# Performance work log

Measured on AMD Instinct MI355X. Metric: run time of the kernel, lower is better.

## Reference

```python
import jax, jax.numpy as jnp
import numpy as np

N, E, B = 50000, 800000, 64
IN, H, OUT = 64, 128, 64


def _gcn_norm(edge_index, num_nodes):
    # PyG gcn_norm with add_self_loops=True: A_hat = A + I, norm = d^-1/2[src]*d^-1/2[dst]
    loop = jnp.arange(num_nodes)
    src = jnp.concatenate([edge_index[0], loop])
    dst = jnp.concatenate([edge_index[1], loop])
    deg = jax.ops.segment_sum(jnp.ones_like(dst, dtype=jnp.float32), dst,
                              num_segments=num_nodes)  # >= 1 due to self-loops
    dis = deg ** -0.5
    norm = dis[src] * dis[dst]  # [E+N]
    return src, dst, norm


def _gcn_layer(x, W, b, src, dst, norm, num_nodes):
    h = x @ W                                   # linear first (GCNConv order)
    msg = h[src] * norm[:, None]                # gather + normalize, [E+N, H]
    out = jax.ops.segment_sum(msg, dst, num_segments=num_nodes)  # scatter-add
    return out + b


def setup_inputs() -> dict:
    key = jax.random.key(0)
    ks = jax.random.split(key, 12)
    x = jax.random.normal(ks[0], (N, IN), dtype=jnp.float32)
    edge_index = jax.random.randint(ks[1], (2, E), 0, N, dtype=jnp.int64)
    batch = jnp.sort(jax.random.randint(ks[2], (N,), 0, B, dtype=jnp.int64))

    def lin(k, fan_in, fan_out):
        s = 1.0 / np.sqrt(fan_in)
        return jax.random.uniform(k, (fan_in, fan_out), jnp.float32, -s, s)

    return {
        "x": x, "edge_index": edge_index, "batch": batch,
        "W1": lin(ks[3], IN, H), "b1": jnp.zeros((H,), jnp.float32),
        "W2": lin(ks[4], H, H),  "b2": jnp.zeros((H,), jnp.float32),
        "W3": lin(ks[5], H, H),  "b3": jnp.zeros((H,), jnp.float32),
        "W4": lin(ks[6], H, OUT), "b4": jnp.zeros((OUT,), jnp.float32),
    }


def reference(x, edge_index, batch, W1, b1, W2, b2, W3, b3, W4, b4):
    src, dst, norm = _gcn_norm(edge_index, N)
    h = jax.nn.relu(_gcn_layer(x, W1, b1, src, dst, norm, N))
    h = jax.nn.relu(_gcn_layer(h, W2, b2, src, dst, norm, N))
    # global mean pool over graphs
    sums = jax.ops.segment_sum(h, batch, num_segments=B)          # [B, H]
    cnts = jax.ops.segment_sum(jnp.ones((N,), jnp.float32), batch, num_segments=B)
    pooled = sums / jnp.maximum(cnts, 1.0)[:, None]
    # MLP head
    return jax.nn.relu(pooled @ W3 + b3) @ W4 + b4                # [B, OUT]
```

## Files before the change

### kernel.cpp

```cpp
#include <hip/hip_runtime.h>


__device__ __forceinline__ float ldf(const void* p, long long i, int f32) {
    if (f32) return ((const float*)p)[i];
    unsigned int u = ((const unsigned short*)p)[i];
    return __uint_as_float(u << 16);
}
__device__ __forceinline__ float bfl(unsigned int u) { return __uint_as_float(u << 16); }
__device__ __forceinline__ float bfh(unsigned int u) { return __uint_as_float(u & 0xFFFF0000u); }
__device__ __forceinline__ int ld_idx(const int* p, long long i, int i64) {
    return i64 ? p[2 * i] : p[i];
}
__device__ __forceinline__ unsigned short f2bf(float v) {
    unsigned int x = __float_as_uint(v);
    return (unsigned short)((x + 0x7FFFu + ((x >> 16) & 1u)) >> 16);
}
__device__ __forceinline__ int clampi(int v, int lo, int hi) {
    return v < lo ? lo : (v > hi ? hi : v);
}

#define OW1 0
#define OB1 8192
#define OW2 8320
#define OB2 24704
#define OW3 24832
#define OB3 41216
#define OW4 41344
#define OB4 49536
#define OTOT 49600


__global__ void gnn_prep(const void* W1, const void* b1, const void* W2, const void* b2,
                         const void* W3, const void* b3, const void* W4, const void* b4,
                         const void* x, const int* __restrict__ ei,
                         int* __restrict__ flags_out,
                         int* __restrict__ degcnt, float* __restrict__ pooled,
                         float* __restrict__ wsW, unsigned short* __restrict__ xb,
                         int N, int B) {
    __shared__ int s_cnt, s_or;
    const int t = threadIdx.x;
    if (t == 0) { s_cnt = 0; s_or = 0; }
    __syncthreads();
    {
        const unsigned int* w1w = (const unsigned int*)W1;
        int c = 0, o = 0;
        for (int i = t; i < 512; i += 256) {
            unsigned int e = (w1w[i] >> 7) & 0xFFu;
            if (e >= 100 && e <= 140) c++;
        }
        for (int i = t; i < 1024; i += 256) o |= ei[2 * i + 1];
        atomicAdd(&s_cnt, c);
        atomicOr(&s_or, o);
    }
    __syncthreads();
    const int f32 = (s_cnt > 256) ? 0 : 1;
    if (blockIdx.x == 0 && t == 0) {
        flags_out[0] = f32;
        flags_out[1] = (s_or == 0) ? 1 : 0;
    }
    const int i = blockIdx.x * 256 + t;
    const int stride = gridDim.x * 256;
    for (int j = i; j < N; j += stride) degcnt[j] = 0;
    for (int j = i; j < B * 128; j += stride) pooled[j] = 0.f;
    for (int j = i; j < OTOT; j += stride) {
        float v;
        if      (j < OB1) v = ldf(W1, j - OW1, f32);
        else if (j < OW2) v = ldf(b1, j - OB1, f32);
        else if (j < OB2) v = ldf(W2, j - OW2, f32);
        else if (j < OW3) v = ldf(b2, j - OB2, f32);
        else if (j < OB3) v = ldf(W3, j - OW3, f32);
        else if (j < OW4) v = ldf(b3, j - OB3, f32);
        else if (j < OB4) v = ldf(W4, j - OW4, f32);
        else              v = ldf(b4, j - OB4, f32);
        wsW[j] = v;
    }
    if (f32) {
        const float* xf = (const float*)x;
        for (int j = i; j < N * 64; j += stride) xb[j] = f2bf(xf[j]);
    }
}


__global__ void gnn_hist(const int* __restrict__ ei, int E, int N,
                         const int* __restrict__ flags, int* __restrict__ degcnt,
                         int* __restrict__ rank) {
    int base = (blockIdx.x * 256 + threadIdx.x) * 4;
    if (base >= E) return;
    int i64 = flags[1];
    int m = min(4, E - base);
    int d[4], r[4];
#pragma unroll
    for (int j = 0; j < 4; ++j)
        if (j < m) d[j] = clampi(ld_idx(ei, (long long)E + base + j, i64), 0, N - 1);
#pragma unroll
    for (int j = 0; j < 4; ++j)
        if (j < m) r[j] = atomicAdd(&degcnt[d[j]], 1);
#pragma unroll
    for (int j = 0; j < 4; ++j)
        if (j < m) rank[base + j] = r[j];
}

__global__ void gnn_scan1(const int* __restrict__ cnt, int* __restrict__ excl,
                          int* __restrict__ sums, float* __restrict__ dis, int N) {
    __shared__ int sh[256];
    int t = threadIdx.x;
    int i = blockIdx.x * 256 + t;
    int v = (i < N) ? cnt[i] : 0;
    sh[t] = v;
    __syncthreads();
    for (int off = 1; off < 256; off <<= 1) {
        int a = (t >= off) ? sh[t - off] : 0;
        __syncthreads();
        sh[t] += a;
        __syncthreads();
    }
    if (i < N) {
        excl[i] = sh[t] - v;
        dis[i] = rsqrtf((float)v + 1.0f);
    }
    if (t == 255) sums[blockIdx.x] = sh[255];
}

__global__ void gnn_scan2(int* __restrict__ sums, int nb) {
    __shared__ int sh[256];
    int t = threadIdx.x;
    int v = (t < nb) ? sums[t] : 0;
    sh[t] = v;
    __syncthreads();
    for (int off = 1; off < 256; off <<= 1) {
        int a = (t >= off) ? sh[t - off] : 0;
        __syncthreads();
        sh[t] += a;
        __syncthreads();
    }
    if (t < nb) sums[t] = sh[t] - v;
}

template <bool SMALLN>
__global__ void gnn_fill(const int* __restrict__ ei, const int* __restrict__ excl,
                         const int* __restrict__ bsums, const int* __restrict__ rank,
                         void* __restrict__ csr, int E, int N,
                         const int* __restrict__ flags) {
    int e = blockIdx.x * 256 + threadIdx.x;
    if (e >= E) return;
    int i64 = flags[1];
    int s = clampi(ld_idx(ei, (long long)e, i64), 0, N - 1);
    int d = clampi(ld_idx(ei, (long long)E + e, i64), 0, N - 1);
    int pos = excl[d] + bsums[d >> 8] + rank[e];
    if (SMALLN) ((unsigned short*)csr)[pos] = (unsigned short)s;
    else        ((int*)csr)[pos] = s;
}

template <bool SMALLN>
__device__ __forceinline__ int csr_at(const void* csr, int e) {
    return SMALLN ? (int)((const unsigned short*)csr)[e] : ((const int*)csr)[e];
}


template <bool SMALLN>
__global__ __launch_bounds__(128) void gnn_aggx_lin1(const void* __restrict__ x,
                                                     const unsigned short* __restrict__ xconv,
                                                     const int* __restrict__ excl,
                                                     const int* __restrict__ bsums,
                                                     const void* __restrict__ csr,
                                                     const float* __restrict__ dis,
                                                     const int* __restrict__ flags,
                                                     const float* __restrict__ Wf,
                                                     const float* __restrict__ bias,
                                                     int N, int E, float* __restrict__ out) {
    __shared__ float Xs[16 * 64];
    const unsigned int* tab = flags[0] ? (const unsigned int*)xconv : (const unsigned int*)x;
    const int t = threadIdx.x;
    const int nbase = blockIdx.x * 16;
    const int lane = t & 63;
    const int fl = lane & 31;

#pragma unroll
    for (int pass = 0; pass < 4; ++pass) {
        int ln = pass * 4 + (t >> 6) * 2 + (lane >> 5);
        int n = nbase + ln;
        float a0 = 0.f, a1 = 0.f;
        if (n < N) {
            float dn = dis[n], dn2 = dn * dn;
            unsigned int us = tab[(long long)n * 32 + fl];
            a0 = bfl(us) * dn2; a1 = bfh(us) * dn2;
            int beg = excl[n] + bsums[n >> 8];
            int end = (n + 1 < N) ? (excl[n + 1] + bsums[(n + 1) >> 8]) : E;
            int e = beg;
            for (; e + 8 <= end; e += 8) {
                int s0 = csr_at<SMALLN>(csr, e),     s1 = csr_at<SMALLN>(csr, e + 1);
                int s2 = csr_at<SMALLN>(csr, e + 2), s3 = csr_at<SMALLN>(csr, e + 3);
                int s4 = csr_at<SMALLN>(csr, e + 4), s5 = csr_at<SMALLN>(csr, e + 5);
                int s6 = csr_at<SMALLN>(csr, e + 6), s7 = csr_at<SMALLN>(csr, e + 7);
                float w0 = dis[s0], w1 = dis[s1], w2 = dis[s2], w3 = dis[s3];
                float w4 = dis[s4], w5 = dis[s5], w6 = dis[s6], w7 = dis[s7];
                unsigned int u0 = tab[(long long)s0 * 32 + fl];
                unsigned int u1 = tab[(long long)s1 * 32 + fl];
                unsigned int u2 = tab[(long long)s2 * 32 + fl];
                unsigned int u3 = tab[(long long)s3 * 32 + fl];
                unsigned int u4 = tab[(long long)s4 * 32 + fl];
                unsigned int u5 = tab[(long long)s5 * 32 + fl];
                unsigned int u6 = tab[(long long)s6 * 32 + fl];
                unsigned int u7 = tab[(long long)s7 * 32 + fl];
                w0 *= dn; w1 *= dn; w2 *= dn; w3 *= dn;
                w4 *= dn; w5 *= dn; w6 *= dn; w7 *= dn;
                a0 = fmaf(w0, bfl(u0), a0); a1 = fmaf(w0, bfh(u0), a1);
                a0 = fmaf(w1, bfl(u1), a0); a1 = fmaf(w1, bfh(u1), a1);
                a0 = fmaf(w2, bfl(u2), a0); a1 = fmaf(w2, bfh(u2), a1);
                a0 = fmaf(w3, bfl(u3), a0); a1 = fmaf(w3, bfh(u3), a1);
                a0 = fmaf(w4, bfl(u4), a0); a1 = fmaf(w4, bfh(u4), a1);
                a0 = fmaf(w5, bfl(u5), a0); a1 = fmaf(w5, bfh(u5), a1);
                a0 = fmaf(w6, bfl(u6), a0); a1 = fmaf(w6, bfh(u6), a1);
                a0 = fmaf(w7, bfl(u7), a0); a1 = fmaf(w7, bfh(u7), a1);
            }
            for (; e + 4 <= end; e += 4) {
                int s0 = csr_at<SMALLN>(csr, e),     s1 = csr_at<SMALLN>(csr, e + 1);
                int s2 = csr_at<SMALLN>(csr, e + 2), s3 = csr_at<SMALLN>(csr, e + 3);
                float w0 = dis[s0], w1 = dis[s1], w2 = dis[s2], w3 = dis[s3];
                unsigned int u0 = tab[(long long)s0 * 32 + fl];
                unsigned int u1 = tab[(long long)s1 * 32 + fl];
                unsigned int u2 = tab[(long long)s2 * 32 + fl];
                unsigned int u3 = tab[(long long)s3 * 32 + fl];
                w0 *= dn; w1 *= dn; w2 *= dn; w3 *= dn;
                a0 = fmaf(w0, bfl(u0), a0); a1 = fmaf(w0, bfh(u0), a1);
                a0 = fmaf(w1, bfl(u1), a0); a1 = fmaf(w1, bfh(u1), a1);
                a0 = fmaf(w2, bfl(u2), a0); a1 = fmaf(w2, bfh(u2), a1);
                a0 = fmaf(w3, bfl(u3), a0); a1 = fmaf(w3, bfh(u3), a1);
            }
            for (; e < end; ++e) {
                int s = csr_at<SMALLN>(csr, e);
                float w = dis[s] * dn;
                unsigned int u = tab[(long long)s * 32 + fl];
                a0 = fmaf(w, bfl(u), a0); a1 = fmaf(w, bfh(u), a1);
            }
        }
        Xs[ln * 64 + fl * 2]     = a0;
        Xs[ln * 64 + fl * 2 + 1] = a1;
    }
    __syncthreads();

    const int fg = t & 31, ng = t >> 5;
    const int f0 = fg * 4, n0 = ng * 4;
    const float4* Xs4 = (const float4*)Xs;
    const float4* Wp  = (const float4*)Wf;
    float4 acc[4];
#pragma unroll
    for (int j = 0; j < 4; ++j) acc[j] = make_float4(0.f, 0.f, 0.f, 0.f);
#pragma unroll 4
    for (int k4 = 0; k4 < 16; ++k4) {
        const float4 wa = Wp[(4 * k4 + 0) * 32 + fg];
        const float4 wb = Wp[(4 * k4 + 1) * 32 + fg];
        const float4 wc = Wp[(4 * k4 + 2) * 32 + fg];
        const float4 wd = Wp[(4 * k4 + 3) * 32 + fg];
#pragma unroll
        for (int j = 0; j < 4; ++j) {
            const float4 xv = Xs4[(n0 + j) * 16 + k4];
            acc[j].x = fmaf(xv.x, wa.x, acc[j].x); acc[j].y = fmaf(xv.x, wa.y, acc[j].y);
            acc[j].z = fmaf(xv.x, wa.z, acc[j].z); acc[j].w = fmaf(xv.x, wa.w, acc[j].w);
            acc[j].x = fmaf(xv.y, wb.x, acc[j].x); acc[j].y = fmaf(xv.y, wb.y, acc[j].y);
            acc[j].z = fmaf(xv.y, wb.z, acc[j].z); acc[j].w = fmaf(xv.y, wb.w, acc[j].w);
            acc[j].x = fmaf(xv.z, wc.x, acc[j].x); acc[j].y = fmaf(xv.z, wc.y, acc[j].y);
            acc[j].z = fmaf(xv.z, wc.z, acc[j].z); acc[j].w = fmaf(xv.z, wc.w, acc[j].w);
            acc[j].x = fmaf(xv.w, wd.x, acc[j].x); acc[j].y = fmaf(xv.w, wd.y, acc[j].y);
            acc[j].z = fmaf(xv.w, wd.z, acc[j].z); acc[j].w = fmaf(xv.w, wd.w, acc[j].w);
        }
    }
    const float4 b = *(const float4*)&bias[f0];
#pragma unroll
    for (int j = 0; j < 4; ++j) {
        int n = nbase + n0 + j;
        if (n >= N) continue;
        float4 a = acc[j];
        a.x = fmaxf(a.x + b.x, 0.f);
        a.y = fmaxf(a.y + b.y, 0.f);
        a.z = fmaxf(a.z + b.z, 0.f);
        a.w = fmaxf(a.w + b.w, 0.f);
        *(float4*)(out + (long long)n * 128 + f0) = a;
    }
}


template <int K, bool RELU, bool OUTBF>
__global__ __launch_bounds__(128) void gnn_linear(const float* __restrict__ X,
                                                  const float* __restrict__ Wf,
                                                  const float* __restrict__ bias,
                                                  int N, void* __restrict__ out) {
    __shared__ float Xs[16 * K];
    const int t = threadIdx.x;
    const int nbase = blockIdx.x * 16;

#pragma unroll
    for (int it = 0; it < K / 32; ++it) {
        int i4 = t + it * 128;
        int n = nbase + (i4 * 4) / K;
        float4 v = make_float4(0.f, 0.f, 0.f, 0.f);
        if (n < N) v = ((const float4*)X)[(long long)nbase * (K / 4) + i4];
        ((float4*)Xs)[i4] = v;
    }
    __syncthreads();

    const int fg = t & 31, ng = t >> 5;
    const int f0 = fg * 4, n0 = ng * 4;
    const float4* Xs4 = (const float4*)Xs;
    const float4* Wp  = (const float4*)Wf;
    float4 acc[4];
#pragma unroll
    for (int j = 0; j < 4; ++j) acc[j] = make_float4(0.f, 0.f, 0.f, 0.f);
#pragma unroll 4
    for (int k4 = 0; k4 < K / 4; ++k4) {
        const float4 wa = Wp[(4 * k4 + 0) * 32 + fg];
        const float4 wb = Wp[(4 * k4 + 1) * 32 + fg];
        const float4 wc = Wp[(4 * k4 + 2) * 32 + fg];
        const float4 wd = Wp[(4 * k4 + 3) * 32 + fg];
#pragma unroll
        for (int j = 0; j < 4; ++j) {
            const float4 xv = Xs4[(n0 + j) * (K / 4) + k4];
            acc[j].x = fmaf(xv.x, wa.x, acc[j].x); acc[j].y = fmaf(xv.x, wa.y, acc[j].y);
            acc[j].z = fmaf(xv.x, wa.z, acc[j].z); acc[j].w = fmaf(xv.x, wa.w, acc[j].w);
            acc[j].x = fmaf(xv.y, wb.x, acc[j].x); acc[j].y = fmaf(xv.y, wb.y, acc[j].y);
            acc[j].z = fmaf(xv.y, wb.z, acc[j].z); acc[j].w = fmaf(xv.y, wb.w, acc[j].w);
            acc[j].x = fmaf(xv.z, wc.x, acc[j].x); acc[j].y = fmaf(xv.z, wc.y, acc[j].y);
            acc[j].z = fmaf(xv.z, wc.z, acc[j].z); acc[j].w = fmaf(xv.z, wc.w, acc[j].w);
            acc[j].x = fmaf(xv.w, wd.x, acc[j].x); acc[j].y = fmaf(xv.w, wd.y, acc[j].y);
            acc[j].z = fmaf(xv.w, wd.z, acc[j].z); acc[j].w = fmaf(xv.w, wd.w, acc[j].w);
        }
    }
#pragma unroll
    for (int j = 0; j < 4; ++j) {
        int n = nbase + n0 + j;
        if (n >= N) continue;
        float4 a = acc[j];
        if (RELU) {
            const float4 b = *(const float4*)&bias[f0];
            a.x = fmaxf(a.x + b.x, 0.f);
            a.y = fmaxf(a.y + b.y, 0.f);
            a.z = fmaxf(a.z + b.z, 0.f);
            a.w = fmaxf(a.w + b.w, 0.f);
        }
        if (OUTBF) {
            uint2 u;
            u.x = (unsigned int)f2bf(a.x) | ((unsigned int)f2bf(a.y) << 16);
            u.y = (unsigned int)f2bf(a.z) | ((unsigned int)f2bf(a.w) << 16);
            *(uint2*)((unsigned short*)out + (long long)n * 128 + f0) = u;
        } else {
            *(float4*)((float*)out + (long long)n * 128 + f0) = a;
        }
    }
}


template <bool SMALLN>
__global__ __launch_bounds__(256) void gnn_agg_bf(const unsigned short* __restrict__ A2,
                                                  const int* __restrict__ excl,
                                                  const int* __restrict__ bsums,
                                                  const void* __restrict__ csr,
                                                  const float* __restrict__ dis,
                                                  const float* __restrict__ bias,
                                                  float* __restrict__ outC, int N, int E) {
    int t = threadIdx.x;
    int lane = t & 63;
    int n = blockIdx.x * 8 + (t >> 6) * 2 + (lane >> 5);
    if (n >= N) return;
    int fl = lane & 31;
    float dn = dis[n];
    float dn2 = dn * dn;
    uint2 us = *(const uint2*)(A2 + (long long)n * 128 + fl * 4);
    float a0 = bfl(us.x) * dn2, a1 = bfh(us.x) * dn2;
    float a2 = bfl(us.y) * dn2, a3 = bfh(us.y) * dn2;
    int beg = excl[n] + bsums[n >> 8];
    int end = (n + 1 < N) ? (excl[n + 1] + bsums[(n + 1) >> 8]) : E;
    int e = beg;
    for (; e + 8 <= end; e += 8) {
        int s0 = csr_at<SMALLN>(csr, e),     s1 = csr_at<SMALLN>(csr, e + 1);
        int s2 = csr_at<SMALLN>(csr, e + 2), s3 = csr_at<SMALLN>(csr, e + 3);
        int s4 = csr_at<SMALLN>(csr, e + 4), s5 = csr_at<SMALLN>(csr, e + 5);
        int s6 = csr_at<SMALLN>(csr, e + 6), s7 = csr_at<SMALLN>(csr, e + 7);
        float w0 = dis[s0], w1 = dis[s1], w2 = dis[s2], w3 = dis[s3];
        float w4 = dis[s4], w5 = dis[s5], w6 = dis[s6], w7 = dis[s7];
        uint2 u0 = *(const uint2*)(A2 + (long long)s0 * 128 + fl * 4);
        uint2 u1 = *(const uint2*)(A2 + (long long)s1 * 128 + fl * 4);
        uint2 u2 = *(const uint2*)(A2 + (long long)s2 * 128 + fl * 4);
        uint2 u3 = *(const uint2*)(A2 + (long long)s3 * 128 + fl * 4);
        uint2 u4 = *(const uint2*)(A2 + (long long)s4 * 128 + fl * 4);
        uint2 u5 = *(const uint2*)(A2 + (long long)s5 * 128 + fl * 4);
        uint2 u6 = *(const uint2*)(A2 + (long long)s6 * 128 + fl * 4);
        uint2 u7 = *(const uint2*)(A2 + (long long)s7 * 128 + fl * 4);
        w0 *= dn; w1 *= dn; w2 *= dn; w3 *= dn;
        w4 *= dn; w5 *= dn; w6 *= dn; w7 *= dn;
        a0 = fmaf(w0, bfl(u0.x), a0); a1 = fmaf(w0, bfh(u0.x), a1);
        a2 = fmaf(w0, bfl(u0.y), a2); a3 = fmaf(w0, bfh(u0.y), a3);
        a0 = fmaf(w1, bfl(u1.x), a0); a1 = fmaf(w1, bfh(u1.x), a1);
        a2 = fmaf(w1, bfl(u1.y), a2); a3 = fmaf(w1, bfh(u1.y), a3);
        a0 = fmaf(w2, bfl(u2.x), a0); a1 = fmaf(w2, bfh(u2.x), a1);
        a2 = fmaf(w2, bfl(u2.y), a2); a3 = fmaf(w2, bfh(u2.y), a3);
        a0 = fmaf(w3, bfl(u3.x), a0); a1 = fmaf(w3, bfh(u3.x), a1);
        a2 = fmaf(w3, bfl(u3.y), a2); a3 = fmaf(w3, bfh(u3.y), a3);
        a0 = fmaf(w4, bfl(u4.x), a0); a1 = fmaf(w4, bfh(u4.x), a1);
        a2 = fmaf(w4, bfl(u4.y), a2); a3 = fmaf(w4, bfh(u4.y), a3);
        a0 = fmaf(w5, bfl(u5.x), a0); a1 = fmaf(w5, bfh(u5.x), a1);
        a2 = fmaf(w5, bfl(u5.y), a2); a3 = fmaf(w5, bfh(u5.y), a3);
        a0 = fmaf(w6, bfl(u6.x), a0); a1 = fmaf(w6, bfh(u6.x), a1);
        a2 = fmaf(w6, bfl(u6.y), a2); a3 = fmaf(w6, bfh(u6.y), a3);
        a0 = fmaf(w7, bfl(u7.x), a0); a1 = fmaf(w7, bfh(u7.x), a1);
        a2 = fmaf(w7, bfl(u7.y), a2); a3 = fmaf(w7, bfh(u7.y), a3);
    }
    for (; e + 4 <= end; e += 4) {
        int s0 = csr_at<SMALLN>(csr, e),     s1 = csr_at<SMALLN>(csr, e + 1);
        int s2 = csr_at<SMALLN>(csr, e + 2), s3 = csr_at<SMALLN>(csr, e + 3);
        float w0 = dis[s0], w1 = dis[s1], w2 = dis[s2], w3 = dis[s3];
        uint2 u0 = *(const uint2*)(A2 + (long long)s0 * 128 + fl * 4);
        uint2 u1 = *(const uint2*)(A2 + (long long)s1 * 128 + fl * 4);
        uint2 u2 = *(const uint2*)(A2 + (long long)s2 * 128 + fl * 4);
        uint2 u3 = *(const uint2*)(A2 + (long long)s3 * 128 + fl * 4);
        w0 *= dn; w1 *= dn; w2 *= dn; w3 *= dn;
        a0 = fmaf(w0, bfl(u0.x), a0); a1 = fmaf(w0, bfh(u0.x), a1);
        a2 = fmaf(w0, bfl(u0.y), a2); a3 = fmaf(w0, bfh(u0.y), a3);
        a0 = fmaf(w1, bfl(u1.x), a0); a1 = fmaf(w1, bfh(u1.x), a1);
        a2 = fmaf(w1, bfl(u1.y), a2); a3 = fmaf(w1, bfh(u1.y), a3);
        a0 = fmaf(w2, bfl(u2.x), a0); a1 = fmaf(w2, bfh(u2.x), a1);
        a2 = fmaf(w2, bfl(u2.y), a2); a3 = fmaf(w2, bfh(u2.y), a3);
        a0 = fmaf(w3, bfl(u3.x), a0); a1 = fmaf(w3, bfh(u3.x), a1);
        a2 = fmaf(w3, bfl(u3.y), a2); a3 = fmaf(w3, bfh(u3.y), a3);
    }
    for (; e < end; ++e) {
        int s = csr_at<SMALLN>(csr, e);
        float w = dis[s] * dn;
        uint2 u = *(const uint2*)(A2 + (long long)s * 128 + fl * 4);
        a0 = fmaf(w, bfl(u.x), a0); a1 = fmaf(w, bfh(u.x), a1);
        a2 = fmaf(w, bfl(u.y), a2); a3 = fmaf(w, bfh(u.y), a3);
    }
    const float4 b = *(const float4*)&bias[fl * 4];
    float4 o;
    o.x = fmaxf(a0 + b.x, 0.f);
    o.y = fmaxf(a1 + b.y, 0.f);
    o.z = fmaxf(a2 + b.z, 0.f);
    o.w = fmaxf(a3 + b.w, 0.f);
    *(float4*)(outC + (long long)n * 128 + fl * 4) = o;
}


#define PSTRIP 32
__global__ __launch_bounds__(128) void gnn_pool(const float* __restrict__ h,
                                                const int* __restrict__ batch,
                                                const int* __restrict__ flags,
                                                float* __restrict__ pooled, int N, int B) {
    int i64 = flags[1];
    int f = threadIdx.x;
    int n0 = blockIdx.x * PSTRIP;
    if (n0 >= N) return;
    int nend = min(n0 + PSTRIP, N);
    int cur = clampi(ld_idx(batch, n0, i64), 0, B - 1);
    float acc = 0.0f;
    for (int n = n0; n < nend; ++n) {
        int b = clampi(ld_idx(batch, n, i64), 0, B - 1);
        if (b != cur) {
            atomicAdd(&pooled[cur * 128 + f], acc);
            acc = 0.0f; cur = b;
        }
        acc += h[(long long)n * 128 + f];
    }
    atomicAdd(&pooled[cur * 128 + f], acc);
}


__global__ __launch_bounds__(128) void gnn_head(const float* __restrict__ pooled,
                                                const int* __restrict__ batch,
                                                const float* __restrict__ W3,
                                                const float* __restrict__ b3,
                                                const float* __restrict__ W4,
                                                const float* __restrict__ b4,
                                                const int* __restrict__ flags,
                                                void* __restrict__ outv, int N) {
    __shared__ float xs[128];
    __shared__ float rs[128];
    __shared__ float cinv;
    int b = blockIdx.x, f = threadIdx.x;
    if (f == 0) {
        int i64 = flags[1];
        int L = 0, R = N;
        while (L < R) { int m = (L + R) >> 1; if (ld_idx(batch, m, i64) < b) L = m + 1; else R = m; }
        int lo = L;
        L = 0; R = N;
        while (L < R) { int m = (L + R) >> 1; if (ld_idx(batch, m, i64) < b + 1) L = m + 1; else R = m; }
        cinv = 1.0f / fmaxf((float)(L - lo), 1.0f);
    }
    __syncthreads();
    xs[f] = pooled[b * 128 + f] * cinv;
    __syncthreads();
    float acc = b3[f];
    for (int k = 0; k < 128; ++k) acc = fmaf(xs[k], W3[k * 128 + f], acc);
    rs[f] = fmaxf(acc, 0.f);
    __syncthreads();
    if (f < 64) {
        float a2 = b4[f];
        for (int k = 0; k < 128; ++k) a2 = fmaf(rs[k], W4[k * 64 + f], a2);
        if (flags[0]) ((float*)outv)[b * 64 + f] = a2;
        else          ((unsigned short*)outv)[b * 64 + f] = f2bf(a2);
    }
}


extern "C" void kernel_launch(void* const* d_in, const int* in_sizes, int n_in,
                              void* d_out, int out_size, void* d_ws, size_t ws_size,
                              hipStream_t stream) {
    const void* x  = d_in[0];
    const int* ei  = (const int*)d_in[1];
    const int* bat = (const int*)d_in[2];

    const int N = in_sizes[0] / 64;
    const int E = in_sizes[1] / 2;
    const int B = out_size / 64;
    const bool smalln = (N < 65536);

    char* p = (char*)d_ws;
    auto alloc = [&](size_t bytes) { void* q = (void*)p; p += (bytes + 255) & ~(size_t)255; return q; };
    int*   flags    = (int*)alloc(256);
    float* wsW      = (float*)alloc((size_t)OTOT * 4);
    int*   degcnt   = (int*)alloc((size_t)N * 4);
    float* dis      = (float*)alloc((size_t)N * 4);
    int*   excl     = (int*)alloc((size_t)N * 4);
    int*   bsums    = (int*)alloc(1024);
    int*   rank     = (int*)alloc((size_t)E * 4);
    void*  csr      = alloc((size_t)E * (smalln ? 2 : 4));
    unsigned short* xb = (unsigned short*)alloc((size_t)N * 64 * 2);
    float* H1       = (float*)alloc((size_t)N * 128 * 4);
    float* C2       = (float*)alloc((size_t)N * 128 * 4);
    unsigned short* A2 = (unsigned short*)alloc((size_t)N * 128 * 2);
    float* pooled   = (float*)alloc((size_t)B * 128 * 4);
    (void)ws_size; (void)n_in;

    const int nbN = (N + 255) / 256;

    gnn_prep<<<512, 256, 0, stream>>>(d_in[3], d_in[4], d_in[5], d_in[6],
                                      d_in[7], d_in[8], d_in[9], d_in[10],
                                      x, ei, flags, degcnt, pooled, wsW, xb, N, B);

    gnn_hist<<<(E + 1023) / 1024, 256, 0, stream>>>(ei, E, N, flags, degcnt, rank);
    gnn_scan1<<<nbN, 256, 0, stream>>>(degcnt, excl, bsums, dis, N);
    gnn_scan2<<<1, 256, 0, stream>>>(bsums, nbN);
    if (smalln)
        gnn_fill<true><<<(E + 255) / 256, 256, 0, stream>>>(ei, excl, bsums, rank, csr, E, N, flags);
    else
        gnn_fill<false><<<(E + 255) / 256, 256, 0, stream>>>(ei, excl, bsums, rank, csr, E, N, flags);

    const int nlin = (N + 15) / 16;
    const int nagg = (N + 7) / 8;

    if (smalln)
        gnn_aggx_lin1<true><<<nlin, 128, 0, stream>>>(x, xb, excl, bsums, csr, dis, flags,
                                                      wsW + OW1, wsW + OB1, N, E, H1);
    else
        gnn_aggx_lin1<false><<<nlin, 128, 0, stream>>>(x, xb, excl, bsums, csr, dis, flags,
                                                       wsW + OW1, wsW + OB1, N, E, H1);

    gnn_linear<128, false, true><<<nlin, 128, 0, stream>>>(H1, wsW + OW2, wsW + OB2, N, (void*)A2);
    if (smalln)
        gnn_agg_bf<true><<<nagg, 256, 0, stream>>>(A2, excl, bsums, csr, dis, wsW + OB2, C2, N, E);
    else
        gnn_agg_bf<false><<<nagg, 256, 0, stream>>>(A2, excl, bsums, csr, dis, wsW + OB2, C2, N, E);

    gnn_pool<<<(N + PSTRIP - 1) / PSTRIP, 128, 0, stream>>>(C2, bat, flags, pooled, N, B);
    gnn_head<<<B, 128, 0, stream>>>(pooled, bat, wsW + OW3, wsW + OB3,
                                    wsW + OW4, wsW + OB4, flags, d_out, N);
}
```

Before: 272.8 us.

## Pre-scale source rows by inverse sqrt degree and parallelize edge gathers across lanes

Source features are now multiplied by dis[src] once per node: during x-to-bf16 conversion in the fill kernel, and in the layer-2 linear epilogue. The aggregation kernels can then sum plain rows and apply dis[dst] once at the end, which removes the per-edge dis[s] gather and multiply. The aggregation loops now split edges across lane groups with 16-byte vector loads, then combine partial sums with xor shuffles, which gives more memory-level parallelism per node. Rounding the pre-scaled values to bf16 changes numerics slightly, and the x conversion now runs unconditionally inside the fill kernel.

```diff
diff --git a/kernel.cpp b/kernel.cpp
--- a/kernel.cpp
+++ b/kernel.cpp
@@ -32,11 +32,10 @@
 
 __global__ void gnn_prep(const void* W1, const void* b1, const void* W2, const void* b2,
                          const void* W3, const void* b3, const void* W4, const void* b4,
-                         const void* x, const int* __restrict__ ei,
+                         const int* __restrict__ ei,
                          int* __restrict__ flags_out,
                          int* __restrict__ degcnt, float* __restrict__ pooled,
-                         float* __restrict__ wsW, unsigned short* __restrict__ xb,
-                         int N, int B) {
+                         float* __restrict__ wsW, int N, int B) {
     __shared__ int s_cnt, s_or;
     const int t = threadIdx.x;
     if (t == 0) { s_cnt = 0; s_or = 0; }
@@ -74,10 +73,6 @@
         else              v = ldf(b4, j - OB4, f32);
         wsW[j] = v;
     }
-    if (f32) {
-        const float* xf = (const float*)x;
-        for (int j = i; j < N * 64; j += stride) xb[j] = f2bf(xf[j]);
-    }
 }
 
 
@@ -140,15 +135,37 @@
 __global__ void gnn_fill(const int* __restrict__ ei, const int* __restrict__ excl,
                          const int* __restrict__ bsums, const int* __restrict__ rank,
                          void* __restrict__ csr, int E, int N,
-                         const int* __restrict__ flags) {
-    int e = blockIdx.x * 256 + threadIdx.x;
-    if (e >= E) return;
-    int i64 = flags[1];
-    int s = clampi(ld_idx(ei, (long long)e, i64), 0, N - 1);
-    int d = clampi(ld_idx(ei, (long long)E + e, i64), 0, N - 1);
-    int pos = excl[d] + bsums[d >> 8] + rank[e];
-    if (SMALLN) ((unsigned short*)csr)[pos] = (unsigned short)s;
-    else        ((int*)csr)[pos] = s;
+                         const int* __restrict__ flags,
+                         const void* __restrict__ x, const float* __restrict__ dis,
+                         unsigned short* __restrict__ xb) {
+    const int tid = blockIdx.x * 256 + threadIdx.x;
+    const int i64 = flags[1];
+    if (tid < E) {
+        int s = clampi(ld_idx(ei, (long long)tid, i64), 0, N - 1);
+        int d = clampi(ld_idx(ei, (long long)E + tid, i64), 0, N - 1);
+        int pos = excl[d] + bsums[d >> 8] + rank[tid];
+        if (SMALLN) ((unsigned short*)csr)[pos] = (unsigned short)s;
+        else        ((int*)csr)[pos] = s;
+    }
+    const int f32 = flags[0];
+    const int total = N * 16;
+    const int stride = gridDim.x * 256;
+    for (int j = tid; j < total; j += stride) {
+        int n = j >> 4;
+        float dn = dis[n];
+        float v0, v1, v2, v3;
+        if (f32) {
+            float4 xv = ((const float4*)x)[j];
+            v0 = xv.x; v1 = xv.y; v2 = xv.z; v3 = xv.w;
+        } else {
+            ushort4 xv = ((const ushort4*)x)[j];
+            v0 = bfl(xv.x); v1 = bfl(xv.y); v2 = bfl(xv.z); v3 = bfl(xv.w);
+        }
+        ushort4 o;
+        o.x = f2bf(v0 * dn); o.y = f2bf(v1 * dn);
+        o.z = f2bf(v2 * dn); o.w = f2bf(v3 * dn);
+        ((ushort4*)xb)[j] = o;
+    }
 }
 
 template <bool SMALLN>
@@ -158,89 +175,62 @@
 
 
 template <bool SMALLN>
-__global__ __launch_bounds__(128) void gnn_aggx_lin1(const void* __restrict__ x,
-                                                     const unsigned short* __restrict__ xconv,
+__global__ __launch_bounds__(128) void gnn_aggx_lin1(const unsigned short* __restrict__ xb,
                                                      const int* __restrict__ excl,
                                                      const int* __restrict__ bsums,
                                                      const void* __restrict__ csr,
                                                      const float* __restrict__ dis,
-                                                     const int* __restrict__ flags,
                                                      const float* __restrict__ Wf,
                                                      const float* __restrict__ bias,
                                                      int N, int E, float* __restrict__ out) {
     __shared__ float Xs[16 * 64];
-    const unsigned int* tab = flags[0] ? (const unsigned int*)xconv : (const unsigned int*)x;
     const int t = threadIdx.x;
     const int nbase = blockIdx.x * 16;
+    const int wave = t >> 6;
     const int lane = t & 63;
-    const int fl = lane & 31;
-
-#pragma unroll
-    for (int pass = 0; pass < 4; ++pass) {
-        int ln = pass * 4 + (t >> 6) * 2 + (lane >> 5);
-        int n = nbase + ln;
-        float a0 = 0.f, a1 = 0.f;
+    const int eslot = lane >> 3;
+    const int fg = lane & 7;
+
+    for (int pass = 0; pass < 8; ++pass) {
+        const int ln = pass * 2 + wave;
+        const int n = nbase + ln;
+        float a0 = 0.f, a1 = 0.f, a2 = 0.f, a3 = 0.f;
+        float a4 = 0.f, a5 = 0.f, a6 = 0.f, a7 = 0.f;
         if (n < N) {
-            float dn = dis[n], dn2 = dn * dn;
-            unsigned int us = tab[(long long)n * 32 + fl];
-            a0 = bfl(us) * dn2; a1 = bfh(us) * dn2;
             int beg = excl[n] + bsums[n >> 8];
             int end = (n + 1 < N) ? (excl[n + 1] + bsums[(n + 1) >> 8]) : E;
-            int e = beg;
-            for (; e + 8 <= end; e += 8) {
-                int s0 = csr_at<SMALLN>(csr, e),     s1 = csr_at<SMALLN>(csr, e + 1);
-                int s2 = csr_at<SMALLN>(csr, e + 2), s3 = csr_at<SMALLN>(csr, e + 3);
-                int s4 = csr_at<SMALLN>(csr, e + 4), s5 = csr_at<SMALLN>(csr, e + 5);
-                int s6 = csr_at<SMALLN>(csr, e + 6), s7 = csr_at<SMALLN>(csr, e + 7);
-                float w0 = dis[s0], w1 = dis[s1], w2 = dis[s2], w3 = dis[s3];
-                float w4 = dis[s4], w5 = dis[s5], w6 = dis[s6], w7 = dis[s7];
-                unsigned int u0 = tab[(long long)s0 * 32 + fl];
-                unsigned int u1 = tab[(long long)s1 * 32 + fl];
-                unsigned int u2 = tab[(long long)s2 * 32 + fl];
-                unsigned int u3 = tab[(long long)s3 * 32 + fl];
-                unsigned int u4 = tab[(long long)s4 * 32 + fl];
-                unsigned int u5 = tab[(long long)s5 * 32 + fl];
-                unsigned int u6 = tab[(long long)s6 * 32 + fl];
-                unsigned int u7 = tab[(long long)s7 * 32 + fl];
-                w0 *= dn; w1 *= dn; w2 *= dn; w3 *= dn;
-                w4 *= dn; w5 *= dn; w6 *= dn; w7 *= dn;
-                a0 = fmaf(w0, bfl(u0), a0); a1 = fmaf(w0, bfh(u0), a1);
-                a0 = fmaf(w1, bfl(u1), a0); a1 = fmaf(w1, bfh(u1), a1);
-                a0 = fmaf(w2, bfl(u2), a0); a1 = fmaf(w2, bfh(u2), a1);
-                a0 = fmaf(w3, bfl(u3), a0); a1 = fmaf(w3, bfh(u3), a1);
-                a0 = fmaf(w4, bfl(u4), a0); a1 = fmaf(w4, bfh(u4), a1);
-                a0 = fmaf(w5, bfl(u5), a0); a1 = fmaf(w5, bfh(u5), a1);
-                a0 = fmaf(w6, bfl(u6), a0); a1 = fmaf(w6, bfh(u6), a1);
-                a0 = fmaf(w7, bfl(u7), a0); a1 = fmaf(w7, bfh(u7), a1);
+            for (int e = beg + eslot; e < end; e += 8) {
+                int s = csr_at<SMALLN>(csr, e);
+                uint4 u = *(const uint4*)(xb + (long long)s * 64 + fg * 8);
+                a0 += bfl(u.x); a1 += bfh(u.x);
+                a2 += bfl(u.y); a3 += bfh(u.y);
+                a4 += bfl(u.z); a5 += bfh(u.z);
+                a6 += bfl(u.w); a7 += bfh(u.w);
             }
-            for (; e + 4 <= end; e += 4) {
-                int s0 = csr_at<SMALLN>(csr, e),     s1 = csr_at<SMALLN>(csr, e + 1);
-                int s2 = csr_at<SMALLN>(csr, e + 2), s3 = csr_at<SMALLN>(csr, e + 3);
-                float w0 = dis[s0], w1 = dis[s1], w2 = dis[s2], w3 = dis[s3];
-                unsigned int u0 = tab[(long long)s0 * 32 + fl];
-                unsigned int u1 = tab[(long long)s1 * 32 + fl];
-                unsigned int u2 = tab[(long long)s2 * 32 + fl];
-                unsigned int u3 = tab[(long long)s3 * 32 + fl];
-                w0 *= dn; w1 *= dn; w2 *= dn; w3 *= dn;
-                a0 = fmaf(w0, bfl(u0), a0); a1 = fmaf(w0, bfh(u0), a1);
-                a0 = fmaf(w1, bfl(u1), a0); a1 = fmaf(w1, bfh(u1), a1);
-                a0 = fmaf(w2, bfl(u2), a0); a1 = fmaf(w2, bfh(u2), a1);
-                a0 = fmaf(w3, bfl(u3), a0); a1 = fmaf(w3, bfh(u3), a1);
-            }
-            for (; e < end; ++e) {
-                int s = csr_at<SMALLN>(csr, e);
-                float w = dis[s] * dn;
-                unsigned int u = tab[(long long)s * 32 + fl];
-                a0 = fmaf(w, bfl(u), a0); a1 = fmaf(w, bfh(u), a1);
-            }
-        }
-        Xs[ln * 64 + fl * 2]     = a0;
-        Xs[ln * 64 + fl * 2 + 1] = a1;
-    }
-    __syncthreads();
-
-    const int fg = t & 31, ng = t >> 5;
-    const int f0 = fg * 4, n0 = ng * 4;
+        }
+#pragma unroll
+        for (int m = 8; m <= 32; m <<= 1) {
+            a0 += __shfl_xor(a0, m); a1 += __shfl_xor(a1, m);
+            a2 += __shfl_xor(a2, m); a3 += __shfl_xor(a3, m);
+            a4 += __shfl_xor(a4, m); a5 += __shfl_xor(a5, m);
+            a6 += __shfl_xor(a6, m); a7 += __shfl_xor(a7, m);
+        }
+        if (n < N && eslot == 0) {
+            float dn = dis[n];
+            uint4 u = *(const uint4*)(xb + (long long)n * 64 + fg * 8);
+            float4 o0, o1;
+            o0.x = (a0 + bfl(u.x)) * dn; o0.y = (a1 + bfh(u.x)) * dn;
+            o0.z = (a2 + bfl(u.y)) * dn; o0.w = (a3 + bfh(u.y)) * dn;
+            o1.x = (a4 + bfl(u.z)) * dn; o1.y = (a5 + bfh(u.z)) * dn;
+            o1.z = (a6 + bfl(u.w)) * dn; o1.w = (a7 + bfh(u.w)) * dn;
+            *(float4*)&Xs[ln * 64 + fg * 8]     = o0;
+            *(float4*)&Xs[ln * 64 + fg * 8 + 4] = o1;
+        }
+    }
+    __syncthreads();
+
+    const int fgB = t & 31, ng = t >> 5;
+    const int f0 = fgB * 4, n0 = ng * 4;
     const float4* Xs4 = (const float4*)Xs;
     const float4* Wp  = (const float4*)Wf;
     float4 acc[4];
@@ -248,10 +238,10 @@
     for (int j = 0; j < 4; ++j) acc[j] = make_float4(0.f, 0.f, 0.f, 0.f);
 #pragma unroll 4
     for (int k4 = 0; k4 < 16; ++k4) {
-        const float4 wa = Wp[(4 * k4 + 0) * 32 + fg];
-        const float4 wb = Wp[(4 * k4 + 1) * 32 + fg];
-        const float4 wc = Wp[(4 * k4 + 2) * 32 + fg];
-        const float4 wd = Wp[(4 * k4 + 3) * 32 + fg];
+        const float4 wa = Wp[(4 * k4 + 0) * 32 + fgB];
+        const float4 wb = Wp[(4 * k4 + 1) * 32 + fgB];
+        const float4 wc = Wp[(4 * k4 + 2) * 32 + fgB];
+        const float4 wd = Wp[(4 * k4 + 3) * 32 + fgB];
 #pragma unroll
         for (int j = 0; j < 4; ++j) {
             const float4 xv = Xs4[(n0 + j) * 16 + k4];
@@ -284,6 +274,7 @@
 __global__ __launch_bounds__(128) void gnn_linear(const float* __restrict__ X,
                                                   const float* __restrict__ Wf,
                                                   const float* __restrict__ bias,
+                                                  const float* __restrict__ dis,
                                                   int N, void* __restrict__ out) {
     __shared__ float Xs[16 * K];
     const int t = threadIdx.x;
@@ -338,6 +329,8 @@
             a.w = fmaxf(a.w + b.w, 0.f);
         }
         if (OUTBF) {
+            const float dn = dis[n];
+            a.x *= dn; a.y *= dn; a.z *= dn; a.w *= dn;
             uint2 u;
             u.x = (unsigned int)f2bf(a.x) | ((unsigned int)f2bf(a.y) << 16);
             u.y = (unsigned int)f2bf(a.z) | ((unsigned int)f2bf(a.w) << 16);
@@ -357,85 +350,48 @@
                                                   const float* __restrict__ dis,
                                                   const float* __restrict__ bias,
                                                   float* __restrict__ outC, int N, int E) {
-    int t = threadIdx.x;
-    int lane = t & 63;
-    int n = blockIdx.x * 8 + (t >> 6) * 2 + (lane >> 5);
+    const int t = threadIdx.x;
+    const int lane = t & 63;
+    const int n = blockIdx.x * 4 + (t >> 6);
     if (n >= N) return;
-    int fl = lane & 31;
-    float dn = dis[n];
-    float dn2 = dn * dn;
-    uint2 us = *(const uint2*)(A2 + (long long)n * 128 + fl * 4);
-    float a0 = bfl(us.x) * dn2, a1 = bfh(us.x) * dn2;
-    float a2 = bfl(us.y) * dn2, a3 = bfh(us.y) * dn2;
+    const int eslot = lane >> 4;
+    const int fg = lane & 15;
+    float a0 = 0.f, a1 = 0.f, a2 = 0.f, a3 = 0.f;
+    float a4 = 0.f, a5 = 0.f, a6 = 0.f, a7 = 0.f;
     int beg = excl[n] + bsums[n >> 8];
     int end = (n + 1 < N) ? (excl[n + 1] + bsums[(n + 1) >> 8]) : E;
-    int e = beg;
-    for (; e + 8 <= end; e += 8) {
-        int s0 = csr_at<SMALLN>(csr, e),     s1 = csr_at<SMALLN>(csr, e + 1);
-        int s2 = csr_at<SMALLN>(csr, e + 2), s3 = csr_at<SMALLN>(csr, e + 3);
-        int s4 = csr_at<SMALLN>(csr, e + 4), s5 = csr_at<SMALLN>(csr, e + 5);
-        int s6 = csr_at<SMALLN>(csr, e + 6), s7 = csr_at<SMALLN>(csr, e + 7);
-        float w0 = dis[s0], w1 = dis[s1], w2 = dis[s2], w3 = dis[s3];
-        float w4 = dis[s4], w5 = dis[s5], w6 = dis[s6], w7 = dis[s7];
-        uint2 u0 = *(const uint2*)(A2 + (long long)s0 * 128 + fl * 4);
-        uint2 u1 = *(const uint2*)(A2 + (long long)s1 * 128 + fl * 4);
-        uint2 u2 = *(const uint2*)(A2 + (long long)s2 * 128 + fl * 4);
-        uint2 u3 = *(const uint2*)(A2 + (long long)s3 * 128 + fl * 4);
-        uint2 u4 = *(const uint2*)(A2 + (long long)s4 * 128 + fl * 4);
-        uint2 u5 = *(const uint2*)(A2 + (long long)s5 * 128 + fl * 4);
-        uint2 u6 = *(const uint2*)(A2 + (long long)s6 * 128 + fl * 4);
-        uint2 u7 = *(const uint2*)(A2 + (long long)s7 * 128 + fl * 4);
-        w0 *= dn; w1 *= dn; w2 *= dn; w3 *= dn;
-        w4 *= dn; w5 *= dn; w6 *= dn; w7 *= dn;
-        a0 = fmaf(w0, bfl(u0.x), a0); a1 = fmaf(w0, bfh(u0.x), a1);
-        a2 = fmaf(w0, bfl(u0.y), a2); a3 = fmaf(w0, bfh(u0.y), a3);
-        a0 = fmaf(w1, bfl(u1.x), a0); a1 = fmaf(w1, bfh(u1.x), a1);
-        a2 = fmaf(w1, bfl(u1.y), a2); a3 = fmaf(w1, bfh(u1.y), a3);
-        a0 = fmaf(w2, bfl(u2.x), a0); a1 = fmaf(w2, bfh(u2.x), a1);
-        a2 = fmaf(w2, bfl(u2.y), a2); a3 = fmaf(w2, bfh(u2.y), a3);
-        a0 = fmaf(w3, bfl(u3.x), a0); a1 = fmaf(w3, bfh(u3.x), a1);
-        a2 = fmaf(w3, bfl(u3.y), a2); a3 = fmaf(w3, bfh(u3.y), a3);
-        a0 = fmaf(w4, bfl(u4.x), a0); a1 = fmaf(w4, bfh(u4.x), a1);
-        a2 = fmaf(w4, bfl(u4.y), a2); a3 = fmaf(w4, bfh(u4.y), a3);
-        a0 = fmaf(w5, bfl(u5.x), a0); a1 = fmaf(w5, bfh(u5.x), a1);
-        a2 = fmaf(w5, bfl(u5.y), a2); a3 = fmaf(w5, bfh(u5.y), a3);
-        a0 = fmaf(w6, bfl(u6.x), a0); a1 = fmaf(w6, bfh(u6.x), a1);
-        a2 = fmaf(w6, bfl(u6.y), a2); a3 = fmaf(w6, bfh(u6.y), a3);
-        a0 = fmaf(w7, bfl(u7.x), a0); a1 = fmaf(w7, bfh(u7.x), a1);
-        a2 = fmaf(w7, bfl(u7.y), a2); a3 = fmaf(w7, bfh(u7.y), a3);
-    }
-    for (; e + 4 <= end; e += 4) {
-        int s0 = csr_at<SMALLN>(csr, e),     s1 = csr_at<SMALLN>(csr, e + 1);
-        int s2 = csr_at<SMALLN>(csr, e + 2), s3 = csr_at<SMALLN>(csr, e + 3);
-        float w0 = dis[s0], w1 = dis[s1], w2 = dis[s2], w3 = dis[s3];
-        uint2 u0 = *(const uint2*)(A2 + (long long)s0 * 128 + fl * 4);
-        uint2 u1 = *(const uint2*)(A2 + (long long)s1 * 128 + fl * 4);
-        uint2 u2 = *(const uint2*)(A2 + (long long)s2 * 128 + fl * 4);
-        uint2 u3 = *(const uint2*)(A2 + (long long)s3 * 128 + fl * 4);
-        w0 *= dn; w1 *= dn; w2 *= dn; w3 *= dn;
-        a0 = fmaf(w0, bfl(u0.x), a0); a1 = fmaf(w0, bfh(u0.x), a1);
-        a2 = fmaf(w0, bfl(u0.y), a2); a3 = fmaf(w0, bfh(u0.y), a3);
-        a0 = fmaf(w1, bfl(u1.x), a0); a1 = fmaf(w1, bfh(u1.x), a1);
-        a2 = fmaf(w1, bfl(u1.y), a2); a3 = fmaf(w1, bfh(u1.y), a3);
-        a0 = fmaf(w2, bfl(u2.x), a0); a1 = fmaf(w2, bfh(u2.x), a1);
-        a2 = fmaf(w2, bfl(u2.y), a2); a3 = fmaf(w2, bfh(u2.y), a3);
-        a0 = fmaf(w3, bfl(u3.x), a0); a1 = fmaf(w3, bfh(u3.x), a1);
-        a2 = fmaf(w3, bfl(u3.y), a2); a3 = fmaf(w3, bfh(u3.y), a3);
-    }
-    for (; e < end; ++e) {
+    for (int e = beg + eslot; e < end; e += 4) {
         int s = csr_at<SMALLN>(csr, e);
-        float w = dis[s] * dn;
-        uint2 u = *(const uint2*)(A2 + (long long)s * 128 + fl * 4);
-        a0 = fmaf(w, bfl(u.x), a0); a1 = fmaf(w, bfh(u.x), a1);
-        a2 = fmaf(w, bfl(u.y), a2); a3 = fmaf(w, bfh(u.y), a3);
-    }
-    const float4 b = *(const float4*)&bias[fl * 4];
-    float4 o;
-    o.x = fmaxf(a0 + b.x, 0.f);
-    o.y = fmaxf(a1 + b.y, 0.f);
-    o.z = fmaxf(a2 + b.z, 0.f);
-    o.w = fmaxf(a3 + b.w, 0.f);
-    *(float4*)(outC + (long long)n * 128 + fl * 4) = o;
+        uint4 u = *(const uint4*)(A2 + (long long)s * 128 + fg * 8);
+        a0 += bfl(u.x); a1 += bfh(u.x);
+        a2 += bfl(u.y); a3 += bfh(u.y);
+        a4 += bfl(u.z); a5 += bfh(u.z);
+        a6 += bfl(u.w); a7 += bfh(u.w);
+    }
+#pragma unroll
+    for (int m = 16; m <= 32; m <<= 1) {
+        a0 += __shfl_xor(a0, m); a1 += __shfl_xor(a1, m);
+        a2 += __shfl_xor(a2, m); a3 += __shfl_xor(a3, m);
+        a4 += __shfl_xor(a4, m); a5 += __shfl_xor(a5, m);
+        a6 += __shfl_xor(a6, m); a7 += __shfl_xor(a7, m);
+    }
+    if (lane < 16) {
+        float dn = dis[n];
+        uint4 u = *(const uint4*)(A2 + (long long)n * 128 + fg * 8);
+        const float4 bA = *(const float4*)&bias[fg * 8];
+        const float4 bB = *(const float4*)&bias[fg * 8 + 4];
+        float4 o0, o1;
+        o0.x = fmaxf((a0 + bfl(u.x)) * dn + bA.x, 0.f);
+        o0.y = fmaxf((a1 + bfh(u.x)) * dn + bA.y, 0.f);
+        o0.z = fmaxf((a2 + bfl(u.y)) * dn + bA.z, 0.f);
+        o0.w = fmaxf((a3 + bfh(u.y)) * dn + bA.w, 0.f);
+        o1.x = fmaxf((a4 + bfl(u.z)) * dn + bB.x, 0.f);
+        o1.y = fmaxf((a5 + bfh(u.z)) * dn + bB.y, 0.f);
+        o1.z = fmaxf((a6 + bfl(u.w)) * dn + bB.z, 0.f);
+        o1.w = fmaxf((a7 + bfh(u.w)) * dn + bB.w, 0.f);
+        *(float4*)(outC + (long long)n * 128 + fg * 8)     = o0;
+        *(float4*)(outC + (long long)n * 128 + fg * 8 + 4) = o1;
+    }
 }
 
 
@@ -533,27 +489,29 @@
 
     gnn_prep<<<512, 256, 0, stream>>>(d_in[3], d_in[4], d_in[5], d_in[6],
                                       d_in[7], d_in[8], d_in[9], d_in[10],
-                                      x, ei, flags, degcnt, pooled, wsW, xb, N, B);
+                                      ei, flags, degcnt, pooled, wsW, N, B);
 
     gnn_hist<<<(E + 1023) / 1024, 256, 0, stream>>>(ei, E, N, flags, degcnt, rank);
     gnn_scan1<<<nbN, 256, 0, stream>>>(degcnt, excl, bsums, dis, N);
     gnn_scan2<<<1, 256, 0, stream>>>(bsums, nbN);
     if (smalln)
-        gnn_fill<true><<<(E + 255) / 256, 256, 0, stream>>>(ei, excl, bsums, rank, csr, E, N, flags);
+        gnn_fill<true><<<(E + 255) / 256, 256, 0, stream>>>(ei, excl, bsums, rank, csr, E, N,
+                                                            flags, x, dis, xb);
     else
-        gnn_fill<false><<<(E + 255) / 256, 256, 0, stream>>>(ei, excl, bsums, rank, csr, E, N, flags);
+        gnn_fill<false><<<(E + 255) / 256, 256, 0, stream>>>(ei, excl, bsums, rank, csr, E, N,
+                                                             flags, x, dis, xb);
 
     const int nlin = (N + 15) / 16;
-    const int nagg = (N + 7) / 8;
+    const int nagg = (N + 3) / 4;
 
     if (smalln)
-        gnn_aggx_lin1<true><<<nlin, 128, 0, stream>>>(x, xb, excl, bsums, csr, dis, flags,
+        gnn_aggx_lin1<true><<<nlin, 128, 0, stream>>>(xb, excl, bsums, csr, dis,
                                                       wsW + OW1, wsW + OB1, N, E, H1);
     else
-        gnn_aggx_lin1<false><<<nlin, 128, 0, stream>>>(x, xb, excl, bsums, csr, dis, flags,
+        gnn_aggx_lin1<false><<<nlin, 128, 0, stream>>>(xb, excl, bsums, csr, dis,
                                                        wsW + OW1, wsW + OB1, N, E, H1);
 
-    gnn_linear<128, false, true><<<nlin, 128, 0, stream>>>(H1, wsW + OW2, wsW + OB2, N, (void*)A2);
+    gnn_linear<128, false, true><<<nlin, 128, 0, stream>>>(H1, wsW + OW2, wsW + OB2, dis, N, (void*)A2);
     if (smalln)
         gnn_agg_bf<true><<<nagg, 256, 0, stream>>>(A2, excl, bsums, csr, dis, wsW + OB2, C2, N, E);
     else
```

Measured after the change: 278.6 us. 2.1% more time.
